# Performance work log

Hardware: AMD Instinct MI355X
Metric: run time of the kernel (lower is better)

The kernel has to match this reference:

```python
import jax, jax.numpy as jnp
import numpy as np

D_IN = 384
HID = 384
D_OUT = 384

def _kaiming(key, fan_in, fan_out):
    return jax.random.normal(key, (fan_in, fan_out), dtype=jnp.float32) * np.sqrt(2.0 / fan_in)

def setup_inputs() -> dict:
    key = jax.random.key(0)
    ks = jax.random.split(key, 12)
    B, O, T = 8, 1024, 8192
    obj_vecs = jax.random.normal(ks[0], (B, O, D_IN), dtype=jnp.float32)
    pred_vecs = jax.random.normal(ks[1], (B, T, D_IN), dtype=jnp.float32)
    edges = jax.random.randint(ks[2], (B, T, 2), 0, O, dtype=jnp.int64)
    # gconv1: [3D -> H -> 2H + Dout]; gconv2: [H -> H -> Dout]
    w1a = _kaiming(ks[3], 3 * D_IN, HID); b1a = jnp.zeros((HID,), jnp.float32)
    w1b = _kaiming(ks[4], HID, 2 * HID + D_OUT); b1b = jnp.zeros((2 * HID + D_OUT,), jnp.float32)
    w2a = _kaiming(ks[5], HID, HID); b2a = jnp.zeros((HID,), jnp.float32)
    w2b = _kaiming(ks[6], HID, D_OUT); b2b = jnp.zeros((D_OUT,), jnp.float32)
    return {"obj_vecs": obj_vecs, "pred_vecs": pred_vecs, "edges": edges,
            "w1a": w1a, "b1a": b1a, "w1b": w1b, "b1b": b1b,
            "w2a": w2a, "b2a": b2a, "w2b": w2b, "b2b": b2b}

def _gconv_forward(obj_vecs, pred_vecs, edges, w1a, b1a, w1b, b1b, w2a, b2a, w2b, b2b):
    B, O, D = obj_vecs.shape
    s_idx = edges[:, :, 0]  # (B, T)
    o_idx = edges[:, :, 1]
    batch = jnp.arange(B)[:, None]
    subj = obj_vecs[batch, s_idx]  # (B, T, D) gather
    objt = obj_vecs[batch, o_idx]
    triple = jnp.concatenate([subj, pred_vecs, objt], axis=-1)  # (B, T, 3D)
    h = jax.nn.relu(triple @ w1a + b1a)
    t = jax.nn.relu(h @ w1b + b1b)  # (B, T, 2H + Dout)
    new_s = t[:, :, :HID]
    new_p = t[:, :, HID:HID + D_OUT]
    new_o = t[:, :, HID + D_OUT:]
    # scatter_add per batch into (O, H) buffers
    def agg(si, oi, vs, vo):
        return jnp.zeros((O, HID), vs.dtype).at[si].add(vs).at[oi].add(vo)
    pooled = jax.vmap(agg)(s_idx, o_idx, new_s, new_o)  # (B, O, H)
    pooled = pooled / jnp.linalg.norm(pooled)  # global Frobenius norm, as in torch .norm()
    out_obj = jax.nn.relu(jax.nn.relu(pooled @ w2a + b2a) @ w2b + b2b)
    return out_obj, new_p

def reference(obj_vecs, pred_vecs, edges, w1a, b1a, w1b, b1b, w2a, b2a, w2b, b2b):
    return _gconv_forward(obj_vecs, pred_vecs, edges, w1a, b1a, w1b, b1b, w2a, b2a, w2b, b2b)
```

## Files before the change

### kernel.cpp

```cpp
#include <hip/hip_runtime.h>
#include <hip/hip_bf16.h>

#define NB 8
#define NT 8192
#define NO 1024
#define DD 384
#define K1 1152
#define M1 65536
#define MO 8192

typedef __attribute__((ext_vector_type(8))) short bf16x8;
typedef __attribute__((ext_vector_type(4))) float f32x4;
typedef __attribute__((ext_vector_type(4))) unsigned short u16x4;

__device__ __forceinline__ unsigned short f2bf(float f) {
    union { float f; unsigned u; } v; v.f = f;
    unsigned r = v.u + 0x7FFFu + ((v.u >> 16) & 1u);
    return (unsigned short)(r >> 16);
}
__device__ __forceinline__ float bf2f(unsigned short h) {
    union { unsigned u; float f; } v; v.u = ((unsigned)h) << 16;
    return v.f;
}
__device__ __forceinline__ bf16x8 pack8(f32x4 a, f32x4 b) {
    bf16x8 r;
    r[0] = (short)f2bf(a[0]); r[1] = (short)f2bf(a[1]);
    r[2] = (short)f2bf(a[2]); r[3] = (short)f2bf(a[3]);
    r[4] = (short)f2bf(b[0]); r[5] = (short)f2bf(b[1]);
    r[6] = (short)f2bf(b[2]); r[7] = (short)f2bf(b[7-4]);
    r[7] = (short)f2bf(b[3]);
    r[6] = (short)f2bf(b[2]);
    return r;
}
__device__ __forceinline__ void gload16(const void* g, void* l) {
    __builtin_amdgcn_global_load_lds(
        (const __attribute__((address_space(1))) unsigned int*)g,
        (__attribute__((address_space(3))) unsigned int*)l, 16, 0, 0);
}

__global__ void k_cvt4(const float* __restrict__ s, unsigned short* __restrict__ d, int n) {
    int i = (blockIdx.x * blockDim.x + threadIdx.x) * 4;
    if (i >= n) return;
    f32x4 v = *(const f32x4*)(s + i);
    u16x4 o;
    o[0] = f2bf(v[0]); o[1] = f2bf(v[1]); o[2] = f2bf(v[2]); o[3] = f2bf(v[3]);
    *(u16x4*)(d + i) = o;
}
__global__ void k_tr(const float* __restrict__ s, unsigned short* __restrict__ d, int K, int N) {
    int k = blockIdx.x;
    int n = blockIdx.y * blockDim.x + threadIdx.x;
    if (n < N) d[n * K + k] = f2bf(s[k * N + n]);
}

__global__ void k_ss1(const float* __restrict__ p, float* __restrict__ partial, int n4) {
    __shared__ float wsum[4];
    int stride = gridDim.x * blockDim.x;
    float s = 0.f;
    for (int i = blockIdx.x * blockDim.x + threadIdx.x; i < n4; i += stride) {
        f32x4 v = *(const f32x4*)(p + i * 4);
        s += v[0] * v[0] + v[1] * v[1] + v[2] * v[2] + v[3] * v[3];
    }
#pragma unroll
    for (int off = 32; off; off >>= 1) s += __shfl_down(s, off, 64);
    if ((threadIdx.x & 63) == 0) wsum[threadIdx.x >> 6] = s;
    __syncthreads();
    if (threadIdx.x == 0)
        partial[blockIdx.x] = wsum[0] + wsum[1] + wsum[2] + wsum[3];
}
__global__ void k_ss2(const float* __restrict__ partial, float* __restrict__ o) {
    float s = partial[threadIdx.x];
#pragma unroll
    for (int off = 32; off; off >>= 1) s += __shfl_down(s, off, 64);
    __shared__ float w0, w1;
    if (threadIdx.x == 0) w0 = s;
    if (threadIdx.x == 64) w1 = s;
    __syncthreads();
    if (threadIdx.x == 0) o[0] = w0 + w1;
}
__global__ void k_normcvt(const float* __restrict__ p, const float* __restrict__ ss,
                          unsigned short* __restrict__ o) {
    int i = (blockIdx.x * blockDim.x + threadIdx.x) * 8;
    float s = rsqrtf(ss[0]);
    f32x4 a = *(const f32x4*)(p + i), b = *(const f32x4*)(p + i + 4);
    a *= s; b *= s;
    *(bf16x8*)(o + i) = pack8(a, b);
}

__global__ void k_hist(const int* __restrict__ edges, int* __restrict__ cnt) {
    int i = blockIdx.x * 256 + threadIdx.x;
    int2 e = *(const int2*)&edges[(size_t)i * 2];
    int b = i >> 13;
    atomicAdd(&cnt[(b << 10) + e.x], 1);
    atomicAdd(&cnt[(b << 10) + e.y], 1);
}
__global__ void k_scan(const int* __restrict__ cnt, int* __restrict__ offs) {
    __shared__ int a[1024];
    int b = blockIdx.x, t = threadIdx.x;
    int own = cnt[(b << 10) + t];
    a[t] = own;
    __syncthreads();
    for (int s = 1; s < 1024; s <<= 1) {
        int v = (t >= s) ? a[t - s] : 0;
        __syncthreads();
        a[t] += v;
        __syncthreads();
    }
    offs[(b << 10) + t] = a[t] - own;
}
__global__ void k_fill(const int* __restrict__ edges, const int* __restrict__ offs,
                       int* __restrict__ cur, int* __restrict__ elist) {
    int i = blockIdx.x * 256 + threadIdx.x;
    int2 e = *(const int2*)&edges[(size_t)i * 2];
    int b = i >> 13, t = i & (NT - 1);
    int ps = atomicAdd(&cur[(b << 10) + e.x], 1);
    elist[(b << 14) + offs[(b << 10) + e.x] + ps] = t * 2;
    int po = atomicAdd(&cur[(b << 10) + e.y], 1);
    elist[(b << 14) + offs[(b << 10) + e.y] + po] = t * 2 + 1;
}
__global__ void k_pool(const unsigned short* __restrict__ sob, const int* __restrict__ cnt,
                       const int* __restrict__ offs, const int* __restrict__ elist,
                       float* __restrict__ pooled) {
    int w = (blockIdx.x * 256 + threadIdx.x) >> 6;
    int lane = threadIdx.x & 63;
    if (lane >= 48) return;
    int b = w >> 10, o = w & (NO - 1);
    int len = cnt[(b << 10) + o];
    const int* lst = elist + (b << 14) + offs[(b << 10) + o];
    f32x4 a0 = {0.f, 0.f, 0.f, 0.f}, a1 = {0.f, 0.f, 0.f, 0.f};
    f32x4 c0 = {0.f, 0.f, 0.f, 0.f}, c1 = {0.f, 0.f, 0.f, 0.f};
    int j = 0;
    for (; j + 1 < len; j += 2) {
        int e0 = lst[j], e1 = lst[j + 1];
        bf16x8 v0 = *(const bf16x8*)(sob + ((size_t)((b << 13) + (e0 >> 1))) * 768 + (e0 & 1) * DD + lane * 8);
        bf16x8 v1 = *(const bf16x8*)(sob + ((size_t)((b << 13) + (e1 >> 1))) * 768 + (e1 & 1) * DD + lane * 8);
        a0[0] += bf2f((unsigned short)v0[0]); a0[1] += bf2f((unsigned short)v0[1]);
        a0[2] += bf2f((unsigned short)v0[2]); a0[3] += bf2f((unsigned short)v0[3]);
        a1[0] += bf2f((unsigned short)v0[4]); a1[1] += bf2f((unsigned short)v0[5]);
        a1[2] += bf2f((unsigned short)v0[6]); a1[3] += bf2f((unsigned short)v0[7]);
        c0[0] += bf2f((unsigned short)v1[0]); c0[1] += bf2f((unsigned short)v1[1]);
        c0[2] += bf2f((unsigned short)v1[2]); c0[3] += bf2f((unsigned short)v1[3]);
        c1[0] += bf2f((unsigned short)v1[4]); c1[1] += bf2f((unsigned short)v1[5]);
        c1[2] += bf2f((unsigned short)v1[6]); c1[3] += bf2f((unsigned short)v1[7]);
    }
    if (j < len) {
        int e0 = lst[j];
        bf16x8 v0 = *(const bf16x8*)(sob + ((size_t)((b << 13) + (e0 >> 1))) * 768 + (e0 & 1) * DD + lane * 8);
        a0[0] += bf2f((unsigned short)v0[0]); a0[1] += bf2f((unsigned short)v0[1]);
        a0[2] += bf2f((unsigned short)v0[2]); a0[3] += bf2f((unsigned short)v0[3]);
        a1[0] += bf2f((unsigned short)v0[4]); a1[1] += bf2f((unsigned short)v0[5]);
        a1[2] += bf2f((unsigned short)v0[6]); a1[3] += bf2f((unsigned short)v0[7]);
    }
    a0 += c0; a1 += c1;
    float* dst = pooled + ((size_t)((b << 10) + o)) * DD + lane * 8;
    *(f32x4*)dst = a0;
    *(f32x4*)(dst + 4) = a1;
}

__launch_bounds__(512, 1)
__global__ void gemm_g1(const unsigned short* __restrict__ objb,
                        const float* __restrict__ predf,
                        const int* __restrict__ edges,
                        const unsigned short* __restrict__ Bt,
                        const float* __restrict__ bias,
                        unsigned short* __restrict__ outb)
{
    const int tid = threadIdx.x;
    const int lane = tid & 63;
    const int m0 = blockIdx.x * 128;

    __shared__ unsigned short lds[2][32768];

    const int rb = tid >> 3;
    const int c8 = ((tid & 7) ^ (rb & 7)) * 8;

    const int bb = (m0 >> 13) << 10;
    int er0[2], er1[2];
#pragma unroll
    for (int i = 0; i < 2; ++i) {
        int2 e = *(const int2*)&edges[(size_t)(m0 + i * 64 + rb) * 2];
        er0[i] = bb + e.x;
        er1[i] = bb + e.y;
    }

    f32x4 acc[4][6];
#pragma unroll
    for (int i = 0; i < 4; ++i)
#pragma unroll
        for (int j = 0; j < 6; ++j) acc[i][j] = (f32x4){0.f, 0.f, 0.f, 0.f};

    const int wid = tid >> 6, wm = wid >> 2, wn = wid & 3;
    const int l16 = lane & 15, lg = lane >> 4;

#pragma unroll
    for (int i = 0; i < 2; ++i)
        gload16(objb + (size_t)er0[i] * DD + c8, &lds[0][i * 4096 + tid * 8]);
#pragma unroll
    for (int i = 0; i < 6; ++i)
        gload16(Bt + (size_t)(i * 64 + rb) * K1 + c8, &lds[0][8192 + i * 4096 + tid * 8]);

    const int nsteps = K1 / 64;
    for (int t = 0; t < nsteps; ++t) {
        const int cur = t & 1;
        const int tn = t + 1;
        if (tn < nsteps) {
            const int nseg = tn / 6;
            const int ko = (tn - nseg * 6) * 64;
            if (nseg == 1) {
                f32x4 pf[2][2];
#pragma unroll
                for (int i = 0; i < 2; ++i) {
                    const float* p = predf + (size_t)(m0 + i * 64 + rb) * DD + ko + c8;
                    pf[i][0] = *(const f32x4*)p;
                    pf[i][1] = *(const f32x4*)(p + 4);
                }
#pragma unroll
                for (int i = 0; i < 6; ++i)
                    gload16(Bt + (size_t)(i * 64 + rb) * K1 + tn * 64 + c8,
                            &lds[cur ^ 1][8192 + i * 4096 + tid * 8]);
#pragma unroll
                for (int i = 0; i < 2; ++i)
                    *(bf16x8*)(&lds[cur ^ 1][i * 4096 + tid * 8]) = pack8(pf[i][0], pf[i][1]);
            } else {
                const unsigned short* asrc0 = (nseg == 0) ? objb + (size_t)er0[0] * DD + ko + c8
                                                          : objb + (size_t)er1[0] * DD + ko + c8;
                const unsigned short* asrc1 = (nseg == 0) ? objb + (size_t)er0[1] * DD + ko + c8
                                                          : objb + (size_t)er1[1] * DD + ko + c8;
                gload16(asrc0, &lds[cur ^ 1][0 * 4096 + tid * 8]);
                gload16(asrc1, &lds[cur ^ 1][1 * 4096 + tid * 8]);
#pragma unroll
                for (int i = 0; i < 6; ++i)
                    gload16(Bt + (size_t)(i * 64 + rb) * K1 + tn * 64 + c8,
                            &lds[cur ^ 1][8192 + i * 4096 + tid * 8]);
                asm volatile("s_waitcnt vmcnt(8)" ::: "memory");
            }
        } else {
            asm volatile("s_waitcnt vmcnt(0)" ::: "memory");
        }
        __builtin_amdgcn_s_barrier();
        const unsigned short* At = &lds[cur][0];
        const unsigned short* Bl = &lds[cur][8192];
#pragma unroll
        for (int kt = 0; kt < 2; ++kt) {
            const int cs = ((kt * 4 + lg) ^ (l16 & 7)) * 8;
            bf16x8 af[4], bfr[6];
#pragma unroll
            for (int mt = 0; mt < 4; ++mt)
                af[mt] = *(const bf16x8*)(At + (wm * 64 + mt * 16 + l16) * 64 + cs);
#pragma unroll
            for (int nn = 0; nn < 6; ++nn)
                bfr[nn] = *(const bf16x8*)(Bl + (wn * 96 + nn * 16 + l16) * 64 + cs);
#pragma unroll
            for (int mt = 0; mt < 4; ++mt)
#pragma unroll
                for (int nn = 0; nn < 6; ++nn)
                    acc[mt][nn] = __builtin_amdgcn_mfma_f32_16x16x32_bf16(af[mt], bfr[nn], acc[mt][nn], 0, 0, 0);
        }
        asm volatile("s_waitcnt lgkmcnt(0)" ::: "memory");
        __builtin_amdgcn_s_barrier();
    }

#pragma unroll
    for (int nn = 0; nn < 6; ++nn) {
        int gn = wn * 96 + nn * 16 + l16;
        float bv = bias[gn];
#pragma unroll
        for (int mt = 0; mt < 4; ++mt) {
            int rbase = wm * 64 + mt * 16 + lg * 4;
#pragma unroll
            for (int rg = 0; rg < 4; ++rg) {
                int gr = m0 + rbase + rg;
                float v = fmaxf(acc[mt][nn][rg] + bv, 0.0f);
                outb[(size_t)gr * DD + gn] = f2bf(v);
            }
        }
    }
}

template <int EPI>
__launch_bounds__(512, 1)
__global__ void gemm_p(const unsigned short* __restrict__ Abf,
                       const unsigned short* __restrict__ Bt,
                       const float* __restrict__ bias,
                       unsigned short* __restrict__ outb,
                       float* __restrict__ outf,
                       int K, int ldC, int bt0p, int btys, int cstride)
{
    const int tid = threadIdx.x;
    const int lane = tid & 63;
    const int m0 = blockIdx.x * 128;
    const int bt0 = bt0p + (int)blockIdx.y * btys;
    const int col0 = (int)blockIdx.y * cstride;

    __shared__ unsigned short lds[2][32768];

    const int rb = tid >> 3;
    const int c8 = ((tid & 7) ^ (rb & 7)) * 8;

    f32x4 acc[4][6];
#pragma unroll
    for (int i = 0; i < 4; ++i)
#pragma unroll
        for (int j = 0; j < 6; ++j) acc[i][j] = (f32x4){0.f, 0.f, 0.f, 0.f};

    const int wid = tid >> 6, wm = wid >> 2, wn = wid & 3;
    const int l16 = lane & 15, lg = lane >> 4;

#define STAGE_P(BUF, KK)                                                                   \
    {                                                                                      \
        _Pragma("unroll")                                                                  \
        for (int i = 0; i < 6; ++i)                                                        \
            gload16(Bt + (size_t)(bt0 + i * 64 + rb) * K + (KK) + c8,                      \
                    &lds[BUF][8192 + i * 4096 + tid * 8]);                                 \
        _Pragma("unroll")                                                                  \
        for (int i = 0; i < 2; ++i)                                                        \
            gload16(Abf + (size_t)(m0 + i * 64 + rb) * K + (KK) + c8,                      \
                    &lds[BUF][i * 4096 + tid * 8]);                                        \
    }

    const int nt = K / 64;
    STAGE_P(0, 0)
    for (int t = 0; t < nt; ++t) {
        const int cur = t & 1;
        if (t + 1 < nt) {
            STAGE_P(cur ^ 1, (t + 1) * 64)
            asm volatile("s_waitcnt vmcnt(8)" ::: "memory");
        } else {
            asm volatile("s_waitcnt vmcnt(0)" ::: "memory");
        }
        __builtin_amdgcn_s_barrier();
        const unsigned short* At = &lds[cur][0];
        const unsigned short* Bl = &lds[cur][8192];
#pragma unroll
        for (int kt = 0; kt < 2; ++kt) {
            const int cs = ((kt * 4 + lg) ^ (l16 & 7)) * 8;
            bf16x8 af[4], bfr[6];
#pragma unroll
            for (int mt = 0; mt < 4; ++mt)
                af[mt] = *(const bf16x8*)(At + (wm * 64 + mt * 16 + l16) * 64 + cs);
#pragma unroll
            for (int nn = 0; nn < 6; ++nn)
                bfr[nn] = *(const bf16x8*)(Bl + (wn * 96 + nn * 16 + l16) * 64 + cs);
#pragma unroll
            for (int mt = 0; mt < 4; ++mt)
#pragma unroll
                for (int nn = 0; nn < 6; ++nn)
                    acc[mt][nn] = __builtin_amdgcn_mfma_f32_16x16x32_bf16(af[mt], bfr[nn], acc[mt][nn], 0, 0, 0);
        }
        asm volatile("s_waitcnt lgkmcnt(0)" ::: "memory");
        __builtin_amdgcn_s_barrier();
    }
#undef STAGE_P

#pragma unroll
    for (int nn = 0; nn < 6; ++nn) {
        int gn = wn * 96 + nn * 16 + l16;
        float bv = bias[bt0 + gn];
#pragma unroll
        for (int mt = 0; mt < 4; ++mt) {
            int rbase = wm * 64 + mt * 16 + lg * 4;
#pragma unroll
            for (int rg = 0; rg < 4; ++rg) {
                int gr = m0 + rbase + rg;
                float v = fmaxf(acc[mt][nn][rg] + bv, 0.0f);
                if (EPI == 0) outb[(size_t)gr * ldC + col0 + gn] = f2bf(v);
                else          outf[(size_t)gr * ldC + col0 + gn] = v;
            }
        }
    }
}

extern "C" void kernel_launch(void* const* d_in, const int* in_sizes, int n_in,
                              void* d_out, int out_size, void* d_ws, size_t ws_size,
                              hipStream_t stream)
{
    const float* obj  = (const float*)d_in[0];
    const float* pred = (const float*)d_in[1];
    const int* edges  = (const int*)d_in[2];
    const float* w1a  = (const float*)d_in[3];
    const float* b1a  = (const float*)d_in[4];
    const float* w1b  = (const float*)d_in[5];
    const float* b1b  = (const float*)d_in[6];
    const float* w2a  = (const float*)d_in[7];
    const float* b2a  = (const float*)d_in[8];
    const float* w2b  = (const float*)d_in[9];
    const float* b2b  = (const float*)d_in[10];

    float* out_obj = (float*)d_out;
    float* newp    = out_obj + (size_t)MO * DD;
    unsigned short* sob = (unsigned short*)newp;

    unsigned short* objb = (unsigned short*)d_ws;
    unsigned short* w1aT = objb + (size_t)NB * NO * DD;
    unsigned short* w1bT = w1aT + (size_t)DD * K1;
    unsigned short* w2aT = w1bT + (size_t)K1 * DD;
    unsigned short* w2bT = w2aT + (size_t)DD * DD;
    unsigned short* hbuf = w2bT + (size_t)DD * DD;
    float* pooled = (float*)(hbuf + (size_t)M1 * DD);
    float* sumsq  = pooled + (size_t)MO * DD;
    unsigned short* hid2 = (unsigned short*)(sumsq + 4);
    int* cnt   = (int*)(hid2 + (size_t)MO * DD);
    int* cur   = cnt + NB * NO;
    int* offs  = cur + NB * NO;
    int* elist = offs + NB * NO;
    float* partial = (float*)(elist + 2 * M1);
    unsigned short* poolb = objb;

    hipLaunchKernelGGL(k_cvt4, dim3(3072), dim3(256), 0, stream, obj, objb, NB * NO * DD);
    hipLaunchKernelGGL(k_tr, dim3(K1, 3), dim3(128), 0, stream, w1a, w1aT, K1, DD);
    hipLaunchKernelGGL(k_tr, dim3(DD, 9), dim3(128), 0, stream, w1b, w1bT, DD, K1);
    hipLaunchKernelGGL(k_tr, dim3(DD, 3), dim3(128), 0, stream, w2a, w2aT, DD, DD);
    hipLaunchKernelGGL(k_tr, dim3(DD, 3), dim3(128), 0, stream, w2b, w2bT, DD, DD);
    hipMemsetAsync(cnt, 0, 2 * NB * NO * sizeof(int), stream);

    hipLaunchKernelGGL(gemm_g1, dim3(M1 / 128), dim3(512), 0, stream,
                       objb, pred, edges, w1aT, b1a, hbuf);

    hipLaunchKernelGGL((gemm_p<0>), dim3(M1 / 128, 2), dim3(512), 0, stream,
                       hbuf, w1bT, b1b, sob, (float*)nullptr, DD, 2 * DD, 0, 2 * DD, DD);

    hipLaunchKernelGGL(k_hist, dim3(256), dim3(256), 0, stream, edges, cnt);
    hipLaunchKernelGGL(k_scan, dim3(8), dim3(1024), 0, stream, cnt, offs);
    hipLaunchKernelGGL(k_fill, dim3(256), dim3(256), 0, stream, edges, offs, cur, elist);
    hipLaunchKernelGGL(k_pool, dim3(2048), dim3(256), 0, stream, sob, cnt, offs, elist, pooled);

    hipLaunchKernelGGL((gemm_p<2>), dim3(M1 / 128, 1), dim3(512), 0, stream,
                       hbuf, w1bT, b1b, (unsigned short*)nullptr, newp, DD, DD, DD, 0, 0);

    hipLaunchKernelGGL(k_ss1, dim3(128), dim3(256), 0, stream, pooled, partial, MO * DD / 4);
    hipLaunchKernelGGL(k_ss2, dim3(1), dim3(128), 0, stream, partial, sumsq);
    hipLaunchKernelGGL(k_normcvt, dim3(1536), dim3(256), 0, stream, pooled, sumsq, poolb);

    hipLaunchKernelGGL((gemm_p<0>), dim3(MO / 128, 1), dim3(512), 0, stream,
                       poolb, w2aT, b2a, hid2, (float*)nullptr, DD, DD, 0, 0, 0);

    hipLaunchKernelGGL((gemm_p<2>), dim3(MO / 128, 1), dim3(512), 0, stream,
                       hid2, w2bT, b2b, (unsigned short*)nullptr, out_obj, DD, DD, 0, 0, 0);
}
```

Measured before the change: 274.4 us.

## Single-buffer B tile in LDS to cut shared memory and raise occupancy

Both GEMM kernels now double-buffer only the A tile and keep a single B tile. The next B tile is loaded after the post-compute barrier, which shrinks LDS per block from 128KB to 80KB. Launch bounds go from 1 to 4 blocks per CU so more waves can hide latency. The cost is that B loads are no longer overlapped with the compute of the previous step, and a single 80KB block per CU still limits real occupancy, so the higher launch bound may only add register pressure.

```diff
diff --git a/kernel.cpp b/kernel.cpp
--- a/kernel.cpp
+++ b/kernel.cpp
@@ -27,9 +27,7 @@
     r[0] = (short)f2bf(a[0]); r[1] = (short)f2bf(a[1]);
     r[2] = (short)f2bf(a[2]); r[3] = (short)f2bf(a[3]);
     r[4] = (short)f2bf(b[0]); r[5] = (short)f2bf(b[1]);
-    r[6] = (short)f2bf(b[2]); r[7] = (short)f2bf(b[7-4]);
-    r[7] = (short)f2bf(b[3]);
-    r[6] = (short)f2bf(b[2]);
+    r[6] = (short)f2bf(b[2]); r[7] = (short)f2bf(b[3]);
     return r;
 }
 __device__ __forceinline__ void gload16(const void* g, void* l) {
@@ -156,7 +154,7 @@
     *(f32x4*)(dst + 4) = a1;
 }
 
-__launch_bounds__(512, 1)
+__launch_bounds__(512, 4)
 __global__ void gemm_g1(const unsigned short* __restrict__ objb,
                         const float* __restrict__ predf,
                         const int* __restrict__ edges,
@@ -168,7 +166,8 @@
     const int lane = tid & 63;
     const int m0 = blockIdx.x * 128;
 
-    __shared__ unsigned short lds[2][32768];
+    __shared__ unsigned short ldsA[2][8192];
+    __shared__ unsigned short ldsB[24576];
 
     const int rb = tid >> 3;
     const int c8 = ((tid & 7) ^ (rb & 7)) * 8;
@@ -193,10 +192,10 @@
 
 #pragma unroll
     for (int i = 0; i < 2; ++i)
-        gload16(objb + (size_t)er0[i] * DD + c8, &lds[0][i * 4096 + tid * 8]);
+        gload16(objb + (size_t)er0[i] * DD + c8, &ldsA[0][i * 4096 + tid * 8]);
 #pragma unroll
     for (int i = 0; i < 6; ++i)
-        gload16(Bt + (size_t)(i * 64 + rb) * K1 + c8, &lds[0][8192 + i * 4096 + tid * 8]);
+        gload16(Bt + (size_t)(i * 64 + rb) * K1 + c8, &ldsB[i * 4096 + tid * 8]);
 
     const int nsteps = K1 / 64;
     for (int t = 0; t < nsteps; ++t) {
@@ -214,31 +213,23 @@
                     pf[i][1] = *(const f32x4*)(p + 4);
                 }
 #pragma unroll
-                for (int i = 0; i < 6; ++i)
-                    gload16(Bt + (size_t)(i * 64 + rb) * K1 + tn * 64 + c8,
-                            &lds[cur ^ 1][8192 + i * 4096 + tid * 8]);
-#pragma unroll
                 for (int i = 0; i < 2; ++i)
-                    *(bf16x8*)(&lds[cur ^ 1][i * 4096 + tid * 8]) = pack8(pf[i][0], pf[i][1]);
+                    *(bf16x8*)(&ldsA[cur ^ 1][i * 4096 + tid * 8]) = pack8(pf[i][0], pf[i][1]);
             } else {
-                const unsigned short* asrc0 = (nseg == 0) ? objb + (size_t)er0[0] * DD + ko + c8
-                                                          : objb + (size_t)er1[0] * DD + ko + c8;
-                const unsigned short* asrc1 = (nseg == 0) ? objb + (size_t)er0[1] * DD + ko + c8
-                                                          : objb + (size_t)er1[1] * DD + ko + c8;
-                gload16(asrc0, &lds[cur ^ 1][0 * 4096 + tid * 8]);
-                gload16(asrc1, &lds[cur ^ 1][1 * 4096 + tid * 8]);
-#pragma unroll
-                for (int i = 0; i < 6; ++i)
-                    gload16(Bt + (size_t)(i * 64 + rb) * K1 + tn * 64 + c8,
-                            &lds[cur ^ 1][8192 + i * 4096 + tid * 8]);
-                asm volatile("s_waitcnt vmcnt(8)" ::: "memory");
+                const unsigned short* base = (nseg == 0) ? objb : objb;
+#pragma unroll
+                for (int i = 0; i < 2; ++i) {
+                    int row = (nseg == 0) ? er0[i] : er1[i];
+                    gload16(objb + (size_t)row * DD + ko + c8, &ldsA[cur ^ 1][i * 4096 + tid * 8]);
+                }
+                (void)base;
+                asm volatile("s_waitcnt vmcnt(2)" ::: "memory");
             }
         } else {
             asm volatile("s_waitcnt vmcnt(0)" ::: "memory");
         }
         __builtin_amdgcn_s_barrier();
-        const unsigned short* At = &lds[cur][0];
-        const unsigned short* Bl = &lds[cur][8192];
+        const unsigned short* At = &ldsA[cur][0];
 #pragma unroll
         for (int kt = 0; kt < 2; ++kt) {
             const int cs = ((kt * 4 + lg) ^ (l16 & 7)) * 8;
@@ -248,7 +239,7 @@
                 af[mt] = *(const bf16x8*)(At + (wm * 64 + mt * 16 + l16) * 64 + cs);
 #pragma unroll
             for (int nn = 0; nn < 6; ++nn)
-                bfr[nn] = *(const bf16x8*)(Bl + (wn * 96 + nn * 16 + l16) * 64 + cs);
+                bfr[nn] = *(const bf16x8*)(ldsB + (wn * 96 + nn * 16 + l16) * 64 + cs);
 #pragma unroll
             for (int mt = 0; mt < 4; ++mt)
 #pragma unroll
@@ -257,6 +248,11 @@
         }
         asm volatile("s_waitcnt lgkmcnt(0)" ::: "memory");
         __builtin_amdgcn_s_barrier();
+        if (tn < nsteps) {
+#pragma unroll
+            for (int i = 0; i < 6; ++i)
+                gload16(Bt + (size_t)(i * 64 + rb) * K1 + tn * 64 + c8, &ldsB[i * 4096 + tid * 8]);
+        }
     }
 
 #pragma unroll
@@ -277,7 +273,7 @@
 }
 
 template <int EPI>
-__launch_bounds__(512, 1)
+__launch_bounds__(512, 4)
 __global__ void gemm_p(const unsigned short* __restrict__ Abf,
                        const unsigned short* __restrict__ Bt,
                        const float* __restrict__ bias,
@@ -291,7 +287,8 @@
     const int bt0 = bt0p + (int)blockIdx.y * btys;
     const int col0 = (int)blockIdx.y * cstride;
 
-    __shared__ unsigned short lds[2][32768];
+    __shared__ unsigned short ldsA[2][8192];
+    __shared__ unsigned short ldsB[24576];
 
     const int rb = tid >> 3;
     const int c8 = ((tid & 7) ^ (rb & 7)) * 8;
@@ -305,31 +302,28 @@
     const int wid = tid >> 6, wm = wid >> 2, wn = wid & 3;
     const int l16 = lane & 15, lg = lane >> 4;
 
-#define STAGE_P(BUF, KK)                                                                   \
-    {                                                                                      \
-        _Pragma("unroll")                                                                  \
-        for (int i = 0; i < 6; ++i)                                                        \
-            gload16(Bt + (size_t)(bt0 + i * 64 + rb) * K + (KK) + c8,                      \
-                    &lds[BUF][8192 + i * 4096 + tid * 8]);                                 \
-        _Pragma("unroll")                                                                  \
-        for (int i = 0; i < 2; ++i)                                                        \
-            gload16(Abf + (size_t)(m0 + i * 64 + rb) * K + (KK) + c8,                      \
-                    &lds[BUF][i * 4096 + tid * 8]);                                        \
-    }
+#pragma unroll
+    for (int i = 0; i < 2; ++i)
+        gload16(Abf + (size_t)(m0 + i * 64 + rb) * K + c8, &ldsA[0][i * 4096 + tid * 8]);
+#pragma unroll
+    for (int i = 0; i < 6; ++i)
+        gload16(Bt + (size_t)(bt0 + i * 64 + rb) * K + c8, &ldsB[i * 4096 + tid * 8]);
 
     const int nt = K / 64;
-    STAGE_P(0, 0)
     for (int t = 0; t < nt; ++t) {
         const int cur = t & 1;
-        if (t + 1 < nt) {
-            STAGE_P(cur ^ 1, (t + 1) * 64)
-            asm volatile("s_waitcnt vmcnt(8)" ::: "memory");
+        const int tn = t + 1;
+        if (tn < nt) {
+#pragma unroll
+            for (int i = 0; i < 2; ++i)
+                gload16(Abf + (size_t)(m0 + i * 64 + rb) * K + tn * 64 + c8,
+                        &ldsA[cur ^ 1][i * 4096 + tid * 8]);
+            asm volatile("s_waitcnt vmcnt(2)" ::: "memory");
         } else {
             asm volatile("s_waitcnt vmcnt(0)" ::: "memory");
         }
         __builtin_amdgcn_s_barrier();
-        const unsigned short* At = &lds[cur][0];
-        const unsigned short* Bl = &lds[cur][8192];
+        const unsigned short* At = &ldsA[cur][0];
 #pragma unroll
         for (int kt = 0; kt < 2; ++kt) {
             const int cs = ((kt * 4 + lg) ^ (l16 & 7)) * 8;
@@ -339,7 +333,7 @@
                 af[mt] = *(const bf16x8*)(At + (wm * 64 + mt * 16 + l16) * 64 + cs);
 #pragma unroll
             for (int nn = 0; nn < 6; ++nn)
-                bfr[nn] = *(const bf16x8*)(Bl + (wn * 96 + nn * 16 + l16) * 64 + cs);
+                bfr[nn] = *(const bf16x8*)(ldsB + (wn * 96 + nn * 16 + l16) * 64 + cs);
 #pragma unroll
             for (int mt = 0; mt < 4; ++mt)
 #pragma unroll
@@ -348,8 +342,13 @@
         }
         asm volatile("s_waitcnt lgkmcnt(0)" ::: "memory");
         __builtin_amdgcn_s_barrier();
-    }
-#undef STAGE_P
+        if (tn < nt) {
+#pragma unroll
+            for (int i = 0; i < 6; ++i)
+                gload16(Bt + (size_t)(bt0 + i * 64 + rb) * K + tn * 64 + c8,
+                        &ldsB[i * 4096 + tid * 8]);
+        }
+    }
 
 #pragma unroll
     for (int nn = 0; nn < 6; ++nn) {
```

Result: slower. 547.9 us (+99.7%).
